# Kernel tuning notes

Measured on AMD Instinct MI355X. Metric: run time of the kernel, lower is better.

Reference implementation:

```python
import jax, jax.numpy as jnp
import numpy as np

B, L, H, NH = 2, 1024, 768, 12
NE, M, NC, CW = 24, 3, 2, 8
BLOCK, NCLS = 64, 97
OFFSET = 1  # bert cls offset


def setup_inputs() -> dict:
    key = jax.random.key(0)
    ks = jax.random.split(key, 10)
    s = 0.02
    return {
        "sequence_output": jax.random.normal(ks[0], (B, L, H), jnp.float32),
        "attention": jax.random.uniform(ks[1], (B, NH, L, L), jnp.float32),
        "mention_starts": jax.random.randint(ks[2], (B, NE, M), 0, L - 2),
        "coref_starts": jax.random.randint(ks[3], (B, NE, NC), 0, L - CW),
        "W_head": jax.random.normal(ks[4], (H, 2 * H), jnp.float32) * s,
        "b_head": jnp.zeros((H,), jnp.float32),
        "W_tail": jax.random.normal(ks[5], (H, 2 * H), jnp.float32) * s,
        "b_tail": jnp.zeros((H,), jnp.float32),
        "W_proj": jax.random.normal(ks[6], (H, H * BLOCK), jnp.float32) * s,
        "W_cls": jax.random.normal(ks[7], (NCLS, H), jnp.float32) * s,
        "b_cls": jnp.zeros((NCLS,), jnp.float32),
    }


def reference(sequence_output, attention, mention_starts, coref_starts,
              W_head, b_head, W_tail, b_tail, W_proj, W_cls, b_cls):
    # ---- get_hrt (NoGraphConv/NoKGEmbedding => graph feats are zeros; residual=True) ----
    p = mention_starts + OFFSET                              # [B,NE,M]
    bidx = jnp.arange(B)[:, None, None]
    m_emb = sequence_output[bidx, p]                         # [B,NE,M,H]
    # attention[i,:,pos] gathered for every mention -> [B,NE,M,NH,L]
    m_att = attention[bidx, :, p]

    # gated coref: gate_score = mean-over-mentions, sum-over-heads, normalized
    att = m_att.mean(2).sum(2)                               # [B,NE,L]
    gate = att / att.sum(-1, keepdims=True)                  # [B,NE,L]

    widx = coref_starts[..., None] + jnp.arange(CW)          # [B,NE,NC,CW]
    gate_g = jnp.take_along_axis(gate[:, :, None, :], widx, axis=-1)   # [B,NE,NC,CW]
    seq_g = sequence_output[jnp.arange(B)[:, None, None, None], widx]  # [B,NE,NC,CW,H]
    coref_emb = (gate_g[..., None] * seq_g).sum(3)           # [B,NE,NC,H]

    # entity embedding: logsumexp over mentions + gated coref vectors
    e_emb = jax.nn.logsumexp(jnp.concatenate([m_emb, coref_emb], axis=2), axis=2)  # [B,NE,H]
    e_att = m_att.mean(2)                                    # [B,NE,NH,L]

    # head-tail localized context: relu((h_att*t_att).sum(heads)), normalize, mix tokens
    ht = jax.nn.relu(jnp.einsum('behl,bfhl->befl', e_att, e_att))      # [B,NE,NE,L]
    ht = ht / (ht.sum(-1, keepdims=True) + 1e-10)
    rs = jnp.einsum('befl,bld->befd', ht, sequence_output)   # [B,NE,NE,H]

    hs = jnp.broadcast_to(e_emb[:, :, None, :], (B, NE, NE, H))
    ts = jnp.broadcast_to(e_emb[:, None, :, :], (B, NE, NE, H))

    # ---- extractors + grouped bilinear + projection + classifier ----
    zh = jnp.tanh(jnp.concatenate([hs, rs], -1) @ W_head.T + b_head)   # [B,NE,NE,H]
    zt = jnp.tanh(jnp.concatenate([ts, rs], -1) @ W_tail.T + b_tail)
    K = H // BLOCK
    b1 = zh.reshape(B, NE, NE, K, BLOCK)
    b2 = zt.reshape(B, NE, NE, K, BLOCK)
    bl = (b1[..., :, None] * b2[..., None, :]).reshape(B, NE, NE, H * BLOCK)
    feature = bl @ W_proj.T                                  # [B,NE,NE,H] (NoAxialTransformer adds zeros)
    logits = feature @ W_cls.T + b_cls                       # [B,NE,NE,NCLS]
    return logits
```

## Files before the change

### kernel.cpp

```cpp
#include <hip/hip_runtime.h>
#include <math.h>

#define BB   2
#define LL   1024
#define HH   768
#define NHH  12
#define NEE  24
#define MMM  3
#define NCC  2
#define CWW  8
#define BLK  64
#define NCLS 97
#define KB   12
#define HB   49152
#define NCP  128
#define NCT  7
#define NEF  1152

typedef unsigned int uint;
typedef unsigned short ushort;
typedef __attribute__((ext_vector_type(8))) short bf16x8;
typedef __attribute__((ext_vector_type(4))) float f32x4;

__device__ __forceinline__ ushort f2bf(float f) {
    uint u = __float_as_uint(f);
    u += 0x7fffu + ((u >> 16) & 1u);
    return (ushort)(u >> 16);
}

__global__ void k_prep(const float* __restrict__ Wc, ushort* __restrict__ wcpack,
                       float* __restrict__ rs, float* __restrict__ out,
                       const float* __restrict__ bc) {
    int bid = blockIdx.x;
    if (bid < 42) {
        int t = bid * 256 + threadIdx.x;
        if (t >= 24 * NCT * 64) return;
        int kc = t / (NCT * 64);
        int r = t % (NCT * 64);
        int ct = r >> 6;
        int lane = r & 63;
        int c = ct * 16 + (lane & 15);
        int k0 = kc * 32 + (lane >> 4) * 8;
        uint u[4] = {0u, 0u, 0u, 0u};
        if (c < NCLS) {
            const float* src = Wc + (size_t)c * HH + k0;
            float4 f0 = *(const float4*)src;
            float4 f1 = *(const float4*)(src + 4);
            u[0] = (uint)f2bf(f0.x) | ((uint)f2bf(f0.y) << 16);
            u[1] = (uint)f2bf(f0.z) | ((uint)f2bf(f0.w) << 16);
            u[2] = (uint)f2bf(f1.x) | ((uint)f2bf(f1.y) << 16);
            u[3] = (uint)f2bf(f1.z) | ((uint)f2bf(f1.w) << 16);
        }
        *(uint4*)(wcpack + (size_t)t * 8) = make_uint4(u[0], u[1], u[2], u[3]);
    } else if (bid < 42 + 3456) {
        int i = (bid - 42) * 256 + threadIdx.x;
        rs[i] = 0.f;
    } else {
        int i = (bid - 3498) * 256 + threadIdx.x;
        if (i < NEF * NCLS) out[i] = bc[i % NCLS];
    }
}

__global__ void k_head(const float* __restrict__ att_in, const float* __restrict__ seq,
                       const int* __restrict__ ms, const int* __restrict__ cs,
                       float* __restrict__ e_att, float* __restrict__ e_emb) {
    __shared__ float es[NHH][LL];
    __shared__ float gs[LL];
    __shared__ float red[16];
    int be = blockIdx.x;
    int b = be / NEE;
    int base = be * MMM;
    int p0 = ms[base + 0] + 1;
    int p1 = ms[base + 1] + 1;
    int p2 = ms[base + 2] + 1;
    int l = threadIdx.x;
    float* eo = e_att + (size_t)be * NHH * LL;
#pragma unroll
    for (int h = 0; h < NHH; h++) {
        const float* basep = att_in + (size_t)(b * NHH + h) * LL * LL;
        float v = (basep[(size_t)p0 * LL + l] + basep[(size_t)p1 * LL + l] +
                   basep[(size_t)p2 * LL + l]) * (1.f / 3.f);
        es[h][l] = v;
        eo[h * LL + l] = v;
    }
    __syncthreads();
    float a = 0.f;
#pragma unroll
    for (int h = 0; h < NHH; h++) a += es[h][l];
    float s = a;
    for (int off = 32; off; off >>= 1) s += __shfl_down(s, off, 64);
    if ((l & 63) == 0) red[l >> 6] = s;
    __syncthreads();
    float tot = 0.f;
#pragma unroll
    for (int i = 0; i < 16; i++) tot += red[i];
    gs[l] = a * (1.f / tot);
    __syncthreads();
    if (l < HH) {
        int d = l;
        int c0 = cs[be * NCC + 0], c1 = cs[be * NCC + 1];
        float v0 = seq[((size_t)b * LL + p0) * HH + d];
        float v1 = seq[((size_t)b * LL + p1) * HH + d];
        float v2 = seq[((size_t)b * LL + p2) * HH + d];
        float s0 = 0.f, s1 = 0.f;
#pragma unroll
        for (int w = 0; w < CWW; w++) {
            s0 += gs[c0 + w] * seq[((size_t)b * LL + c0 + w) * HH + d];
            s1 += gs[c1 + w] * seq[((size_t)b * LL + c1 + w) * HH + d];
        }
        float mx = fmaxf(fmaxf(fmaxf(v0, v1), fmaxf(v2, s0)), s1);
        float se = expf(v0 - mx) + expf(v1 - mx) + expf(v2 - mx) + expf(s0 - mx) + expf(s1 - mx);
        e_emb[(size_t)be * HH + d] = logf(se) + mx;
    }
}

__global__ void k_ht(const float* __restrict__ e_att, float* __restrict__ ht) {
    int blk = blockIdx.x;
    int f = blk % NEE;
    int e = (blk / NEE) % NEE;
    int b = blk / (NEE * NEE);
    const float* ea = e_att + (size_t)(b * NEE + e) * NHH * LL;
    const float* fa = e_att + (size_t)(b * NEE + f) * NHH * LL;
    __shared__ float hts[LL];
    __shared__ float red[4];
    float lsum = 0.f;
    for (int l = threadIdx.x; l < LL; l += blockDim.x) {
        float s = 0.f;
        for (int h = 0; h < NHH; h++) s += ea[h * LL + l] * fa[h * LL + l];
        s = fmaxf(s, 0.f);
        hts[l] = s;
        lsum += s;
    }
    for (int off = 32; off; off >>= 1) lsum += __shfl_down(lsum, off, 64);
    if ((threadIdx.x & 63) == 0) red[threadIdx.x >> 6] = lsum;
    __syncthreads();
    float inv = 1.f / (red[0] + red[1] + red[2] + red[3] + 1e-10f);
    for (int l = threadIdx.x; l < LL; l += blockDim.x)
        ht[(size_t)blk * LL + l] = hts[l] * inv;
}

__global__ void k_mid(const float* __restrict__ seq, const float* __restrict__ ht,
                      float* __restrict__ rs, const float* __restrict__ e_emb,
                      const float* __restrict__ Wh, const float* __restrict__ Wt,
                      float* __restrict__ hsW, float* __restrict__ tsW) {
    __shared__ float As[16][68], Bs[16][68];
    __shared__ float xs[HH];
    int bid = blockIdx.x;
    if (bid < 432) {
        int m0 = (bid % 9) * 64;
        int n0 = ((bid / 9) % 12) * 64;
        int z  = bid / 108;
        int b  = z >> 1;
        int k0base = (z & 1) * 512;
        const float* A  = ht  + (size_t)b * 576 * 1024;
        const float* Bm = seq + (size_t)b * 1024 * 768;
        float* C = rs + (size_t)b * 576 * 768;
        int tx = threadIdx.x & 15, ty = threadIdx.x >> 4;
        int lr = threadIdx.x >> 2;
        int lk = (threadIdx.x & 3) * 4;
        int kr = threadIdx.x >> 4;
        int c4 = (threadIdx.x & 15) * 4;
        float acc[4][4] = {};
        const float* arow = A + (size_t)(m0 + lr) * 1024 + k0base;
        const float* brow = Bm + (size_t)(k0base + kr) * 768 + n0 + c4;
        for (int k0 = 0; k0 < 512; k0 += 16) {
            float4 av = *(const float4*)(arow + k0 + lk);
            float4 bv = *(const float4*)(brow + (size_t)k0 * 768);
            __syncthreads();
            As[lk + 0][lr] = av.x; As[lk + 1][lr] = av.y; As[lk + 2][lr] = av.z; As[lk + 3][lr] = av.w;
            *(float4*)&Bs[kr][c4] = bv;
            __syncthreads();
#pragma unroll
            for (int kk = 0; kk < 16; kk++) {
                float a0 = As[kk][ty * 4 + 0], a1 = As[kk][ty * 4 + 1];
                float a2 = As[kk][ty * 4 + 2], a3 = As[kk][ty * 4 + 3];
                float b0 = Bs[kk][tx * 4 + 0], b1 = Bs[kk][tx * 4 + 1];
                float b2 = Bs[kk][tx * 4 + 2], b3 = Bs[kk][tx * 4 + 3];
                acc[0][0] += a0 * b0; acc[0][1] += a0 * b1; acc[0][2] += a0 * b2; acc[0][3] += a0 * b3;
                acc[1][0] += a1 * b0; acc[1][1] += a1 * b1; acc[1][2] += a1 * b2; acc[1][3] += a1 * b3;
                acc[2][0] += a2 * b0; acc[2][1] += a2 * b1; acc[2][2] += a2 * b2; acc[2][3] += a2 * b3;
                acc[3][0] += a3 * b0; acc[3][1] += a3 * b1; acc[3][2] += a3 * b2; acc[3][3] += a3 * b3;
            }
        }
#pragma unroll
        for (int i = 0; i < 4; i++)
#pragma unroll
            for (int j = 0; j < 4; j++)
                atomicAdd(&C[(size_t)(m0 + ty * 4 + i) * 768 + n0 + tx * 4 + j], acc[i][j]);
    } else {
        int r = bid - 432;
        int m2 = r % 48;
        int which = (r / 48) & 1;
        int chunk = r / 96;
        const float* Wm = which ? Wt : Wh;
        float* outp = which ? tsW : hsW;
        const float* x = e_emb + (size_t)m2 * HH;
        for (int j = threadIdx.x; j < HH; j += 256) xs[j] = x[j];
        __syncthreads();
        int lane = threadIdx.x & 63, w = threadIdx.x >> 6;
        int d0 = chunk * 64 + w * 16;
#pragma unroll 4
        for (int i = 0; i < 16; i++) {
            int d = d0 + i;
            const float* wr = Wm + (size_t)d * (2 * HH);
            float s = 0.f;
#pragma unroll
            for (int jj = 0; jj < 12; jj++) s += xs[lane + jj * 64] * wr[lane + jj * 64];
            for (int off = 32; off; off >>= 1) s += __shfl_down(s, off, 64);
            if (lane == 0) outp[(size_t)m2 * HH + d] = s;
        }
    }
}

__global__ void k_rsw(const float* __restrict__ rs, const float* __restrict__ Wh,
                      const float* __restrict__ Wt, const float* __restrict__ hsW,
                      const float* __restrict__ tsW, const float* __restrict__ bh,
                      const float* __restrict__ bt, ushort* __restrict__ zb) {
    int m0 = blockIdx.x * 64, n0 = blockIdx.y * 64;
    __shared__ float As[16][68], Bs[16][68];
    int tx = threadIdx.x & 15, ty = threadIdx.x >> 4;
    int lr = threadIdx.x >> 2;
    int lk = (threadIdx.x & 3) * 4;
    float acc[4][4] = {};
    int n = n0 + lr;
    const float* brow = (n < HH) ? (Wh + (size_t)n * (2 * HH) + HH)
                                 : (Wt + (size_t)(n - HH) * (2 * HH) + HH);
    const float* arow = rs + (size_t)(m0 + lr) * HH;
    for (int k0 = 0; k0 < HH; k0 += 16) {
        float4 av = *(const float4*)(arow + k0 + lk);
        float4 bv = *(const float4*)(brow + k0 + lk);
        __syncthreads();
        As[lk + 0][lr] = av.x; As[lk + 1][lr] = av.y; As[lk + 2][lr] = av.z; As[lk + 3][lr] = av.w;
        Bs[lk + 0][lr] = bv.x; Bs[lk + 1][lr] = bv.y; Bs[lk + 2][lr] = bv.z; Bs[lk + 3][lr] = bv.w;
        __syncthreads();
#pragma unroll
        for (int kk = 0; kk < 16; kk++) {
            float a0 = As[kk][ty * 4 + 0], a1 = As[kk][ty * 4 + 1];
            float a2 = As[kk][ty * 4 + 2], a3 = As[kk][ty * 4 + 3];
            float b0 = Bs[kk][tx * 4 + 0], b1 = Bs[kk][tx * 4 + 1];
            float b2 = Bs[kk][tx * 4 + 2], b3 = Bs[kk][tx * 4 + 3];
            acc[0][0] += a0 * b0; acc[0][1] += a0 * b1; acc[0][2] += a0 * b2; acc[0][3] += a0 * b3;
            acc[1][0] += a1 * b0; acc[1][1] += a1 * b1; acc[1][2] += a1 * b2; acc[1][3] += a1 * b3;
            acc[2][0] += a2 * b0; acc[2][1] += a2 * b1; acc[2][2] += a2 * b2; acc[2][3] += a2 * b3;
            acc[3][0] += a3 * b0; acc[3][1] += a3 * b1; acc[3][2] += a3 * b2; acc[3][3] += a3 * b3;
        }
    }
    bool isHead = (n0 < HH);
#pragma unroll
    for (int i = 0; i < 4; i++) {
        int m = m0 + ty * 4 + i;
        int bb = m / 576;
        int rr = m % 576;
        int e = rr / NEE, f = rr % NEE;
        const float* addrow = isHead ? (hsW + (size_t)(bb * NEE + e) * HH)
                                     : (tsW + (size_t)(bb * NEE + f) * HH);
        const float* bias = isHead ? bh : bt;
#pragma unroll
        for (int j = 0; j < 4; j++) {
            int nn = n0 + tx * 4 + j;
            int d = isHead ? nn : (nn - HH);
            float v = tanhf(acc[i][j] + addrow[d] + bias[d]);
            zb[(size_t)m * (2 * HH) + nn] = f2bf(v);
        }
    }
}

__global__ void k_wf(const float* __restrict__ Wp, const ushort* __restrict__ wcpack,
                     ushort* __restrict__ bpack) {
    int tid = threadIdx.x;
    int lane = tid & 63, w = tid >> 6;
    int r16 = lane & 15, tt = lane >> 4;
    int n0 = blockIdx.x * 64 + w * 16;
    const float* ap = Wp + (size_t)(tt * 8) * HB + n0 + r16;
    const uint4* wb = (const uint4*)wcpack;

    f32x4 acc[NCT];
    f32x4 zero = {0.f, 0.f, 0.f, 0.f};
#pragma unroll
    for (int ct = 0; ct < NCT; ct++) acc[ct] = zero;

    for (int kc = 0; kc < 24; kc++) {
        const float* a0 = ap + (size_t)(kc * 32) * HB;
        float f[8];
#pragma unroll
        for (int j = 0; j < 8; j++) f[j] = a0[(size_t)j * HB];
        union { bf16x8 v; uint u[4]; } a;
#pragma unroll
        for (int q = 0; q < 4; q++)
            a.u[q] = (__float_as_uint(f[2 * q]) >> 16) |
                     (__float_as_uint(f[2 * q + 1]) & 0xFFFF0000u);
#pragma unroll
        for (int ct = 0; ct < NCT; ct++) {
            union { uint4 q; bf16x8 v; } b;
            b.q = wb[(size_t)(kc * NCT + ct) * 64 + lane];
            acc[ct] = __builtin_amdgcn_mfma_f32_16x16x32_bf16(a.v, b.v, acc[ct], 0, 0, 0);
        }
    }
#pragma unroll
    for (int ct = 0; ct < NCT; ct++) {
        int c = ct * 16 + r16;
#pragma unroll
        for (int r = 0; r < 4; r++) {
            int n = n0 + tt * 4 + r;
            bpack[((size_t)(n >> 3) * NCP + c) * 8 + (n & 7)] = f2bf(acc[ct][r]);
        }
    }
}

#define ZTP 88
#define ZHP 48
__global__ __launch_bounds__(256, 2) void k_logits(const ushort* __restrict__ zb,
                                                   const ushort* __restrict__ bpack,
                                                   float* __restrict__ out) {
    __shared__ ushort zhs[64 * ZHP];
    __shared__ ushort zts[64 * ZTP];
    __shared__ ushort Bls[16384];
    int m0 = blockIdx.x * 64;
    int kb = blockIdx.y;
    int kg = kb >> 1;
    int ihalf = (kb & 1) * 32;
    int tid = threadIdx.x;
    int lane = tid & 63, w = tid >> 6;
    int tt = lane >> 4, r16 = lane & 15;
    int wm = (w & 1) * 32, wn = (w >> 1) * 64;

    {
        int row = tid >> 2, c8 = (tid & 3) * 16;
        const ushort* src = zb + (size_t)(m0 + row) * 1536 + 768 + kg * 64 + c8;
        uint4 v0 = *(const uint4*)src;
        uint4 v1 = *(const uint4*)(src + 8);
        *(uint4*)&zts[row * ZTP + c8] = v0;
        *(uint4*)&zts[row * ZTP + c8 + 8] = v1;
    }
    {
        int row = tid >> 2, c8 = (tid & 3) * 8;
        const ushort* src = zb + (size_t)(m0 + row) * 1536 + kg * 64 + ihalf + c8;
        *(uint4*)&zhs[row * ZHP + c8] = *(const uint4*)src;
    }

    f32x4 acc[2][4];
    f32x4 zero = {0.f, 0.f, 0.f, 0.f};
#pragma unroll
    for (int t = 0; t < 2; t++)
#pragma unroll
        for (int n = 0; n < 4; n++) acc[t][n] = zero;

    const char* bbase = (const char*)bpack + (size_t)kb * 2048 * 256;
    for (int g = 0; g < 16; g++) {
        __syncthreads();
        const char* sb = bbase + (size_t)g * 32768;
#pragma unroll
        for (int q = 0; q < 8; q++) {
            int off = (q * 4 + w) * 1024;
            __builtin_amdgcn_global_load_lds(
                (const __attribute__((address_space(1))) void*)(sb + off + lane * 16),
                (__attribute__((address_space(3))) void*)((char*)Bls + off),
                16, 0, 0);
        }
        __syncthreads();
#pragma unroll
        for (int ks = 0; ks < 4; ks++) {
            int s = g * 4 + ks;
            int il = s >> 1;
            int j0 = (s & 1) * 32;
            bf16x8 af[2];
#pragma unroll
            for (int t = 0; t < 2; t++) {
                int row = wm + t * 16 + r16;
                float zhf = __uint_as_float((uint)zhs[row * ZHP + il] << 16);
                union { bf16x8 v; uint u[4]; } zt8, a;
                zt8.v = *(const bf16x8*)&zts[row * ZTP + j0 + tt * 8];
#pragma unroll
                for (int q = 0; q < 4; q++) {
                    uint p = zt8.u[q];
                    uint lo = __float_as_uint(__uint_as_float(p << 16) * zhf);
                    uint hi = __float_as_uint(__uint_as_float(p & 0xFFFF0000u) * zhf);
                    a.u[q] = (lo >> 16) | (hi & 0xFFFF0000u);
                }
                af[t] = a.v;
            }
#pragma unroll
            for (int n = 0; n < 4; n++) {
                bf16x8 bf = *(const bf16x8*)&Bls[(size_t)((ks * 4 + tt) * NCP + wn + n * 16 + r16) * 8];
                acc[0][n] = __builtin_amdgcn_mfma_f32_16x16x32_bf16(af[0], bf, acc[0][n], 0, 0, 0);
                acc[1][n] = __builtin_amdgcn_mfma_f32_16x16x32_bf16(af[1], bf, acc[1][n], 0, 0, 0);
            }
        }
    }
    int rbase = (lane >> 4) * 4;
#pragma unroll
    for (int t = 0; t < 2; t++)
#pragma unroll
        for (int n = 0; n < 4; n++) {
            int c = wn + n * 16 + r16;
            if (c < NCLS) {
                int row = m0 + wm + t * 16 + rbase;
#pragma unroll
                for (int r = 0; r < 4; r++)
                    atomicAdd(&out[(size_t)(row + r) * NCLS + c], acc[t][n][r]);
            }
        }
}

extern "C" void kernel_launch(void* const* d_in, const int* in_sizes, int n_in,
                              void* d_out, int out_size, void* d_ws, size_t ws_size,
                              hipStream_t stream) {
    const float* seq  = (const float*)d_in[0];
    const float* attn = (const float*)d_in[1];
    const int*   ms   = (const int*)d_in[2];
    const int*   cs   = (const int*)d_in[3];
    const float* Wh   = (const float*)d_in[4];
    const float* bh   = (const float*)d_in[5];
    const float* Wt   = (const float*)d_in[6];
    const float* bt   = (const float*)d_in[7];
    const float* Wp   = (const float*)d_in[8];
    const float* Wc   = (const float*)d_in[9];
    const float* bc   = (const float*)d_in[10];
    float* out = (float*)d_out;

    float* w     = (float*)d_ws;
    float* e_att = w;
    float* ht    = e_att + 589824;
    float* rs    = ht + 1179648;
    float* eemb  = rs + 884736;
    float* hsW   = eemb + 36864;
    float* tsW   = hsW + 36864;
    ushort* bpack  = (ushort*)w;
    ushort* zb     = (ushort*)(w + 3145728);
    ushort* wcpack = (ushort*)(w + 4030464);

    k_prep<<<3935, 256, 0, stream>>>(Wc, wcpack, rs, out, bc);
    k_head<<<BB * NEE, 1024, 0, stream>>>(attn, seq, ms, cs, e_att, eemb);
    k_ht<<<NEF, 256, 0, stream>>>(e_att, ht);
    k_mid<<<432 + 1152, 256, 0, stream>>>(seq, ht, rs, eemb, Wh, Wt, hsW, tsW);
    k_rsw<<<dim3(NEF / 64, 2 * HH / 64), 256, 0, stream>>>(rs, Wh, Wt, hsW, tsW, bh, bt, zb);
    k_wf<<<HB / 64, 256, 0, stream>>>(Wp, wcpack, bpack);
    k_logits<<<dim3(NEF / 64, 24), 256, 0, stream>>>(zb, bpack, out);
}
```

Baseline: 461.4 us.

## Use split-bf16 MFMA for rs and rsW GEMMs and merge launches

Converts the two fp32 SIMT GEMMs (ht@seq and rs@W2) into MFMA bf16 GEMMs, using a hi/lo bf16 split (three MFMAs per tile) to keep near-fp32 accuracy. A front kernel now produces transposed seq and W2 hi/lo copies, fuses head/gating and prep work, and ht is fused with the Wp·Wc fold kernel, cutting the launch count from seven to five. The atomic split-K in rs is removed. The cost is extra conversion passes, larger workspace traffic for the hi/lo copies, and uncached global loads that are not staged through LDS.

```diff
diff --git a/kernel.cpp b/kernel.cpp
--- a/kernel.cpp
+++ b/kernel.cpp
@@ -11,7 +11,6 @@
 #define CWW  8
 #define BLK  64
 #define NCLS 97
-#define KB   12
 #define HB   49152
 #define NCP  128
 #define NCT  7
@@ -28,12 +27,26 @@
     return (ushort)(u >> 16);
 }
 
-__global__ void k_prep(const float* __restrict__ Wc, ushort* __restrict__ wcpack,
-                       float* __restrict__ rs, float* __restrict__ out,
-                       const float* __restrict__ bc) {
+__device__ __forceinline__ void splitbf(float f, ushort& h, ushort& l) {
+    h = f2bf(f);
+    float hf = __uint_as_float((uint)h << 16);
+    l = f2bf(f - hf);
+}
+
+__global__ void k_front(const float* __restrict__ att_in, const float* __restrict__ seq,
+                        const int* __restrict__ ms, const int* __restrict__ cs,
+                        const float* __restrict__ Wc, const float* __restrict__ Wh,
+                        const float* __restrict__ Wt, const float* __restrict__ bc,
+                        float* __restrict__ e_att, float* __restrict__ e_emb,
+                        ushort* __restrict__ wcpack,
+                        ushort* __restrict__ seqThi, ushort* __restrict__ seqTlo,
+                        ushort* __restrict__ W2hi, ushort* __restrict__ W2lo,
+                        float* __restrict__ out) {
+    __shared__ float sm[13328];
     int bid = blockIdx.x;
+    int tid = threadIdx.x;
     if (bid < 42) {
-        int t = bid * 256 + threadIdx.x;
+        int t = bid * 256 + tid;
         if (t >= 24 * NCT * 64) return;
         int kc = t / (NCT * 64);
         int r = t % (NCT * 64);
@@ -52,152 +65,233 @@
             u[3] = (uint)f2bf(f1.z) | ((uint)f2bf(f1.w) << 16);
         }
         *(uint4*)(wcpack + (size_t)t * 8) = make_uint4(u[0], u[1], u[2], u[3]);
-    } else if (bid < 42 + 3456) {
-        int i = (bid - 42) * 256 + threadIdx.x;
-        rs[i] = 0.f;
+    } else if (bid < 479) {
+        int i = (bid - 42) * 256 + tid;
+        if (i < NEF * NCLS) out[i] = bc[i % NCLS];
+    } else if (bid < 527) {
+        float* es = sm;
+        float* gs = sm + 12288;
+        float* red = sm + 13312;
+        int be = bid - 479;
+        int b = be / NEE;
+        int base = be * MMM;
+        int p0 = ms[base + 0] + 1, p1 = ms[base + 1] + 1, p2 = ms[base + 2] + 1;
+        float* eo = e_att + (size_t)be * NHH * LL;
+        for (int h = 0; h < NHH; h++) {
+            const float* basep = att_in + (size_t)(b * NHH + h) * LL * LL;
+#pragma unroll
+            for (int i = 0; i < 4; i++) {
+                int l = tid + i * 256;
+                float v = (basep[(size_t)p0 * LL + l] + basep[(size_t)p1 * LL + l] +
+                           basep[(size_t)p2 * LL + l]) * (1.f / 3.f);
+                es[h * LL + l] = v;
+                eo[h * LL + l] = v;
+            }
+        }
+        __syncthreads();
+        float part = 0.f;
+#pragma unroll
+        for (int i = 0; i < 4; i++) {
+            int l = tid + i * 256;
+            float a = 0.f;
+#pragma unroll
+            for (int h = 0; h < NHH; h++) a += es[h * LL + l];
+            gs[l] = a;
+            part += a;
+        }
+        for (int off = 32; off; off >>= 1) part += __shfl_down(part, off, 64);
+        if ((tid & 63) == 0) red[tid >> 6] = part;
+        __syncthreads();
+        float inv = 1.f / (red[0] + red[1] + red[2] + red[3]);
+#pragma unroll
+        for (int i = 0; i < 4; i++) gs[tid + i * 256] *= inv;
+        __syncthreads();
+        int c0 = cs[be * NCC + 0], c1 = cs[be * NCC + 1];
+        for (int d = tid; d < HH; d += 256) {
+            float v0 = seq[((size_t)b * LL + p0) * HH + d];
+            float v1 = seq[((size_t)b * LL + p1) * HH + d];
+            float v2 = seq[((size_t)b * LL + p2) * HH + d];
+            float s0 = 0.f, s1 = 0.f;
+#pragma unroll
+            for (int w = 0; w < CWW; w++) {
+                s0 += gs[c0 + w] * seq[((size_t)b * LL + c0 + w) * HH + d];
+                s1 += gs[c1 + w] * seq[((size_t)b * LL + c1 + w) * HH + d];
+            }
+            float mx = fmaxf(fmaxf(fmaxf(v0, v1), fmaxf(v2, s0)), s1);
+            float se = expf(v0 - mx) + expf(v1 - mx) + expf(v2 - mx) + expf(s0 - mx) + expf(s1 - mx);
+            e_emb[(size_t)be * HH + d] = logf(se) + mx;
+        }
+    } else if (bid < 911) {
+        float (*tile)[65] = (float(*)[65])sm;
+        int idx = bid - 527;
+        int b = idx / 192;
+        int rem = idx % 192;
+        int l0 = (rem / 12) * 64;
+        int d0 = (rem % 12) * 64;
+        int dq = tid >> 6, dl = tid & 63;
+#pragma unroll 4
+        for (int r = 0; r < 16; r++) {
+            int l_in = r * 4 + dq;
+            tile[l_in][dl] = seq[((size_t)(b * LL + l0 + l_in)) * HH + d0 + dl];
+        }
+        __syncthreads();
+#pragma unroll 4
+        for (int r = 0; r < 16; r++) {
+            int d_out = r * 4 + dq;
+            float v = tile[dl][d_out];
+            ushort h, l;
+            splitbf(v, h, l);
+            size_t o = ((size_t)(b * HH + d0 + d_out)) * LL + l0 + dl;
+            seqThi[o] = h;
+            seqTlo[o] = l;
+        }
     } else {
-        int i = (bid - 3498) * 256 + threadIdx.x;
-        if (i < NEF * NCLS) out[i] = bc[i % NCLS];
-    }
-}
-
-__global__ void k_head(const float* __restrict__ att_in, const float* __restrict__ seq,
-                       const int* __restrict__ ms, const int* __restrict__ cs,
-                       float* __restrict__ e_att, float* __restrict__ e_emb) {
-    __shared__ float es[NHH][LL];
-    __shared__ float gs[LL];
-    __shared__ float red[16];
-    int be = blockIdx.x;
-    int b = be / NEE;
-    int base = be * MMM;
-    int p0 = ms[base + 0] + 1;
-    int p1 = ms[base + 1] + 1;
-    int p2 = ms[base + 2] + 1;
-    int l = threadIdx.x;
-    float* eo = e_att + (size_t)be * NHH * LL;
-#pragma unroll
-    for (int h = 0; h < NHH; h++) {
-        const float* basep = att_in + (size_t)(b * NHH + h) * LL * LL;
-        float v = (basep[(size_t)p0 * LL + l] + basep[(size_t)p1 * LL + l] +
-                   basep[(size_t)p2 * LL + l]) * (1.f / 3.f);
-        es[h][l] = v;
-        eo[h * LL + l] = v;
-    }
-    __syncthreads();
-    float a = 0.f;
-#pragma unroll
-    for (int h = 0; h < NHH; h++) a += es[h][l];
-    float s = a;
-    for (int off = 32; off; off >>= 1) s += __shfl_down(s, off, 64);
-    if ((l & 63) == 0) red[l >> 6] = s;
-    __syncthreads();
-    float tot = 0.f;
-#pragma unroll
-    for (int i = 0; i < 16; i++) tot += red[i];
-    gs[l] = a * (1.f / tot);
-    __syncthreads();
-    if (l < HH) {
-        int d = l;
-        int c0 = cs[be * NCC + 0], c1 = cs[be * NCC + 1];
-        float v0 = seq[((size_t)b * LL + p0) * HH + d];
-        float v1 = seq[((size_t)b * LL + p1) * HH + d];
-        float v2 = seq[((size_t)b * LL + p2) * HH + d];
-        float s0 = 0.f, s1 = 0.f;
-#pragma unroll
-        for (int w = 0; w < CWW; w++) {
-            s0 += gs[c0 + w] * seq[((size_t)b * LL + c0 + w) * HH + d];
-            s1 += gs[c1 + w] * seq[((size_t)b * LL + c1 + w) * HH + d];
-        }
-        float mx = fmaxf(fmaxf(fmaxf(v0, v1), fmaxf(v2, s0)), s1);
-        float se = expf(v0 - mx) + expf(v1 - mx) + expf(v2 - mx) + expf(s0 - mx) + expf(s1 - mx);
-        e_emb[(size_t)be * HH + d] = logf(se) + mx;
-    }
-}
-
-__global__ void k_ht(const float* __restrict__ e_att, float* __restrict__ ht) {
-    int blk = blockIdx.x;
-    int f = blk % NEE;
-    int e = (blk / NEE) % NEE;
-    int b = blk / (NEE * NEE);
-    const float* ea = e_att + (size_t)(b * NEE + e) * NHH * LL;
-    const float* fa = e_att + (size_t)(b * NEE + f) * NHH * LL;
+        int idx = bid - 911;
+#pragma unroll
+        for (int rr = 0; rr < 4; rr++) {
+            int n = idx * 4 + rr;
+            const float* src = (n < HH) ? (Wh + (size_t)n * (2 * HH) + HH)
+                                        : (Wt + (size_t)(n - HH) * (2 * HH) + HH);
+            for (int k = tid; k < HH; k += 256) {
+                ushort h, l;
+                splitbf(src[k], h, l);
+                W2hi[(size_t)n * HH + k] = h;
+                W2lo[(size_t)n * HH + k] = l;
+            }
+        }
+    }
+}
+
+__global__ void k_htwf(const float* __restrict__ e_att, const float* __restrict__ Wp,
+                       const ushort* __restrict__ wcpack, ushort* __restrict__ hthi,
+                       ushort* __restrict__ htlo, ushort* __restrict__ bpack) {
     __shared__ float hts[LL];
     __shared__ float red[4];
-    float lsum = 0.f;
-    for (int l = threadIdx.x; l < LL; l += blockDim.x) {
-        float s = 0.f;
-        for (int h = 0; h < NHH; h++) s += ea[h * LL + l] * fa[h * LL + l];
-        s = fmaxf(s, 0.f);
-        hts[l] = s;
-        lsum += s;
-    }
-    for (int off = 32; off; off >>= 1) lsum += __shfl_down(lsum, off, 64);
-    if ((threadIdx.x & 63) == 0) red[threadIdx.x >> 6] = lsum;
-    __syncthreads();
-    float inv = 1.f / (red[0] + red[1] + red[2] + red[3] + 1e-10f);
-    for (int l = threadIdx.x; l < LL; l += blockDim.x)
-        ht[(size_t)blk * LL + l] = hts[l] * inv;
-}
-
-__global__ void k_mid(const float* __restrict__ seq, const float* __restrict__ ht,
-                      float* __restrict__ rs, const float* __restrict__ e_emb,
-                      const float* __restrict__ Wh, const float* __restrict__ Wt,
-                      float* __restrict__ hsW, float* __restrict__ tsW) {
-    __shared__ float As[16][68], Bs[16][68];
+    int bid = blockIdx.x;
+    int tid = threadIdx.x;
+    int lane = tid & 63, w = tid >> 6;
+    if (bid < 768) {
+        int r16 = lane & 15, tt = lane >> 4;
+        int n0 = bid * 64 + w * 16;
+        const float* ap = Wp + (size_t)(tt * 8) * HB + n0 + r16;
+        const uint4* wb = (const uint4*)wcpack;
+        f32x4 acc[NCT];
+        f32x4 zero = {0.f, 0.f, 0.f, 0.f};
+#pragma unroll
+        for (int ct = 0; ct < NCT; ct++) acc[ct] = zero;
+        for (int kc = 0; kc < 24; kc++) {
+            const float* a0 = ap + (size_t)(kc * 32) * HB;
+            float f[8];
+#pragma unroll
+            for (int j = 0; j < 8; j++) f[j] = a0[(size_t)j * HB];
+            union { bf16x8 v; uint u[4]; } a;
+#pragma unroll
+            for (int q = 0; q < 4; q++)
+                a.u[q] = (__float_as_uint(f[2 * q]) >> 16) |
+                         (__float_as_uint(f[2 * q + 1]) & 0xFFFF0000u);
+#pragma unroll
+            for (int ct = 0; ct < NCT; ct++) {
+                union { uint4 q; bf16x8 v; } b;
+                b.q = wb[(size_t)(kc * NCT + ct) * 64 + lane];
+                acc[ct] = __builtin_amdgcn_mfma_f32_16x16x32_bf16(a.v, b.v, acc[ct], 0, 0, 0);
+            }
+        }
+#pragma unroll
+        for (int ct = 0; ct < NCT; ct++) {
+            int c = ct * 16 + r16;
+#pragma unroll
+            for (int r = 0; r < 4; r++) {
+                int n = n0 + tt * 4 + r;
+                bpack[((size_t)(n >> 3) * NCP + c) * 8 + (n & 7)] = f2bf(acc[ct][r]);
+            }
+        }
+    } else {
+        int blk = bid - 768;
+        int f = blk % NEE;
+        int e = (blk / NEE) % NEE;
+        int b = blk / (NEE * NEE);
+        const float* ea = e_att + (size_t)(b * NEE + e) * NHH * LL;
+        const float* fa = e_att + (size_t)(b * NEE + f) * NHH * LL;
+        float lsum = 0.f;
+        for (int l = tid; l < LL; l += 256) {
+            float s = 0.f;
+            for (int h = 0; h < NHH; h++) s += ea[h * LL + l] * fa[h * LL + l];
+            s = fmaxf(s, 0.f);
+            hts[l] = s;
+            lsum += s;
+        }
+        for (int off = 32; off; off >>= 1) lsum += __shfl_down(lsum, off, 64);
+        if ((tid & 63) == 0) red[tid >> 6] = lsum;
+        __syncthreads();
+        float inv = 1.f / (red[0] + red[1] + red[2] + red[3] + 1e-10f);
+        for (int l = tid; l < LL; l += 256) {
+            ushort h, lo;
+            splitbf(hts[l] * inv, h, lo);
+            hthi[(size_t)blk * LL + l] = h;
+            htlo[(size_t)blk * LL + l] = lo;
+        }
+    }
+}
+
+__global__ void k_mid(const ushort* __restrict__ seqThi, const ushort* __restrict__ seqTlo,
+                      const ushort* __restrict__ hthi, const ushort* __restrict__ htlo,
+                      const float* __restrict__ e_emb, const float* __restrict__ Wh,
+                      const float* __restrict__ Wt, ushort* __restrict__ rshi,
+                      ushort* __restrict__ rslo, float* __restrict__ hsW,
+                      float* __restrict__ tsW) {
     __shared__ float xs[HH];
     int bid = blockIdx.x;
-    if (bid < 432) {
-        int m0 = (bid % 9) * 64;
-        int n0 = ((bid / 9) % 12) * 64;
-        int z  = bid / 108;
-        int b  = z >> 1;
-        int k0base = (z & 1) * 512;
-        const float* A  = ht  + (size_t)b * 576 * 1024;
-        const float* Bm = seq + (size_t)b * 1024 * 768;
-        float* C = rs + (size_t)b * 576 * 768;
-        int tx = threadIdx.x & 15, ty = threadIdx.x >> 4;
-        int lr = threadIdx.x >> 2;
-        int lk = (threadIdx.x & 3) * 4;
-        int kr = threadIdx.x >> 4;
-        int c4 = (threadIdx.x & 15) * 4;
-        float acc[4][4] = {};
-        const float* arow = A + (size_t)(m0 + lr) * 1024 + k0base;
-        const float* brow = Bm + (size_t)(k0base + kr) * 768 + n0 + c4;
-        for (int k0 = 0; k0 < 512; k0 += 16) {
-            float4 av = *(const float4*)(arow + k0 + lk);
-            float4 bv = *(const float4*)(brow + (size_t)k0 * 768);
-            __syncthreads();
-            As[lk + 0][lr] = av.x; As[lk + 1][lr] = av.y; As[lk + 2][lr] = av.z; As[lk + 3][lr] = av.w;
-            *(float4*)&Bs[kr][c4] = bv;
-            __syncthreads();
-#pragma unroll
-            for (int kk = 0; kk < 16; kk++) {
-                float a0 = As[kk][ty * 4 + 0], a1 = As[kk][ty * 4 + 1];
-                float a2 = As[kk][ty * 4 + 2], a3 = As[kk][ty * 4 + 3];
-                float b0 = Bs[kk][tx * 4 + 0], b1 = Bs[kk][tx * 4 + 1];
-                float b2 = Bs[kk][tx * 4 + 2], b3 = Bs[kk][tx * 4 + 3];
-                acc[0][0] += a0 * b0; acc[0][1] += a0 * b1; acc[0][2] += a0 * b2; acc[0][3] += a0 * b3;
-                acc[1][0] += a1 * b0; acc[1][1] += a1 * b1; acc[1][2] += a1 * b2; acc[1][3] += a1 * b3;
-                acc[2][0] += a2 * b0; acc[2][1] += a2 * b1; acc[2][2] += a2 * b2; acc[2][3] += a2 * b3;
-                acc[3][0] += a3 * b0; acc[3][1] += a3 * b1; acc[3][2] += a3 * b2; acc[3][3] += a3 * b3;
-            }
-        }
-#pragma unroll
-        for (int i = 0; i < 4; i++)
-#pragma unroll
-            for (int j = 0; j < 4; j++)
-                atomicAdd(&C[(size_t)(m0 + ty * 4 + i) * 768 + n0 + tx * 4 + j], acc[i][j]);
+    int tid = threadIdx.x;
+    int lane = tid & 63, w = tid >> 6;
+    if (bid < 216) {
+        int b = bid / 108;
+        int rem = bid % 108;
+        int m0 = (rem / 12) * 64;
+        int n0 = (rem % 12) * 64;
+        int r16 = lane & 15, tt = lane >> 4;
+        const ushort* Ah = hthi + (size_t)(b * 576 + m0 + w * 16 + r16) * LL;
+        const ushort* Al = htlo + (size_t)(b * 576 + m0 + w * 16 + r16) * LL;
+        const ushort* Bh0 = seqThi + (size_t)(b * HH + n0 + r16) * LL;
+        const ushort* Bl0 = seqTlo + (size_t)(b * HH + n0 + r16) * LL;
+        f32x4 acc[4];
+        f32x4 zero = {0.f, 0.f, 0.f, 0.f};
+#pragma unroll
+        for (int nt = 0; nt < 4; nt++) acc[nt] = zero;
+        for (int kc = 0; kc < 32; kc++) {
+            int ko = kc * 32 + tt * 8;
+            bf16x8 ah = *(const bf16x8*)(Ah + ko);
+            bf16x8 al = *(const bf16x8*)(Al + ko);
+#pragma unroll
+            for (int nt = 0; nt < 4; nt++) {
+                bf16x8 bh = *(const bf16x8*)(Bh0 + (size_t)nt * 16 * LL + ko);
+                bf16x8 bl = *(const bf16x8*)(Bl0 + (size_t)nt * 16 * LL + ko);
+                acc[nt] = __builtin_amdgcn_mfma_f32_16x16x32_bf16(ah, bh, acc[nt], 0, 0, 0);
+                acc[nt] = __builtin_amdgcn_mfma_f32_16x16x32_bf16(ah, bl, acc[nt], 0, 0, 0);
+                acc[nt] = __builtin_amdgcn_mfma_f32_16x16x32_bf16(al, bh, acc[nt], 0, 0, 0);
+            }
+        }
+#pragma unroll
+        for (int nt = 0; nt < 4; nt++) {
+#pragma unroll
+            for (int r = 0; r < 4; r++) {
+                int m = b * 576 + m0 + w * 16 + tt * 4 + r;
+                int d = n0 + nt * 16 + r16;
+                ushort h, l;
+                splitbf(acc[nt][r], h, l);
+                rshi[(size_t)m * HH + d] = h;
+                rslo[(size_t)m * HH + d] = l;
+            }
+        }
     } else {
-        int r = bid - 432;
+        int r = bid - 216;
         int m2 = r % 48;
         int which = (r / 48) & 1;
         int chunk = r / 96;
         const float* Wm = which ? Wt : Wh;
         float* outp = which ? tsW : hsW;
         const float* x = e_emb + (size_t)m2 * HH;
-        for (int j = threadIdx.x; j < HH; j += 256) xs[j] = x[j];
-        __syncthreads();
-        int lane = threadIdx.x & 63, w = threadIdx.x >> 6;
+        for (int j = tid; j < HH; j += 256) xs[j] = x[j];
+        __syncthreads();
         int d0 = chunk * 64 + w * 16;
 #pragma unroll 4
         for (int i = 0; i < 16; i++) {
@@ -212,97 +306,52 @@
     }
 }
 
-__global__ void k_rsw(const float* __restrict__ rs, const float* __restrict__ Wh,
-                      const float* __restrict__ Wt, const float* __restrict__ hsW,
-                      const float* __restrict__ tsW, const float* __restrict__ bh,
-                      const float* __restrict__ bt, ushort* __restrict__ zb) {
+__global__ void k_rsw(const ushort* __restrict__ rshi, const ushort* __restrict__ rslo,
+                      const ushort* __restrict__ W2hi, const ushort* __restrict__ W2lo,
+                      const float* __restrict__ hsW, const float* __restrict__ tsW,
+                      const float* __restrict__ bh, const float* __restrict__ bt,
+                      ushort* __restrict__ zb) {
     int m0 = blockIdx.x * 64, n0 = blockIdx.y * 64;
-    __shared__ float As[16][68], Bs[16][68];
-    int tx = threadIdx.x & 15, ty = threadIdx.x >> 4;
-    int lr = threadIdx.x >> 2;
-    int lk = (threadIdx.x & 3) * 4;
-    float acc[4][4] = {};
-    int n = n0 + lr;
-    const float* brow = (n < HH) ? (Wh + (size_t)n * (2 * HH) + HH)
-                                 : (Wt + (size_t)(n - HH) * (2 * HH) + HH);
-    const float* arow = rs + (size_t)(m0 + lr) * HH;
-    for (int k0 = 0; k0 < HH; k0 += 16) {
-        float4 av = *(const float4*)(arow + k0 + lk);
-        float4 bv = *(const float4*)(brow + k0 + lk);
-        __syncthreads();
-        As[lk + 0][lr] = av.x; As[lk + 1][lr] = av.y; As[lk + 2][lr] = av.z; As[lk + 3][lr] = av.w;
-        Bs[lk + 0][lr] = bv.x; Bs[lk + 1][lr] = bv.y; Bs[lk + 2][lr] = bv.z; Bs[lk + 3][lr] = bv.w;
-        __syncthreads();
-#pragma unroll
-        for (int kk = 0; kk < 16; kk++) {
-            float a0 = As[kk][ty * 4 + 0], a1 = As[kk][ty * 4 + 1];
-            float a2 = As[kk][ty * 4 + 2], a3 = As[kk][ty * 4 + 3];
-            float b0 = Bs[kk][tx * 4 + 0], b1 = Bs[kk][tx * 4 + 1];
-            float b2 = Bs[kk][tx * 4 + 2], b3 = Bs[kk][tx * 4 + 3];
-            acc[0][0] += a0 * b0; acc[0][1] += a0 * b1; acc[0][2] += a0 * b2; acc[0][3] += a0 * b3;
-            acc[1][0] += a1 * b0; acc[1][1] += a1 * b1; acc[1][2] += a1 * b2; acc[1][3] += a1 * b3;
-            acc[2][0] += a2 * b0; acc[2][1] += a2 * b1; acc[2][2] += a2 * b2; acc[2][3] += a2 * b3;
-            acc[3][0] += a3 * b0; acc[3][1] += a3 * b1; acc[3][2] += a3 * b2; acc[3][3] += a3 * b3;
-        }
-    }
-    bool isHead = (n0 < HH);
-#pragma unroll
-    for (int i = 0; i < 4; i++) {
-        int m = m0 + ty * 4 + i;
-        int bb = m / 576;
-        int rr = m % 576;
-        int e = rr / NEE, f = rr % NEE;
-        const float* addrow = isHead ? (hsW + (size_t)(bb * NEE + e) * HH)
-                                     : (tsW + (size_t)(bb * NEE + f) * HH);
-        const float* bias = isHead ? bh : bt;
-#pragma unroll
-        for (int j = 0; j < 4; j++) {
-            int nn = n0 + tx * 4 + j;
-            int d = isHead ? nn : (nn - HH);
-            float v = tanhf(acc[i][j] + addrow[d] + bias[d]);
-            zb[(size_t)m * (2 * HH) + nn] = f2bf(v);
-        }
-    }
-}
-
-__global__ void k_wf(const float* __restrict__ Wp, const ushort* __restrict__ wcpack,
-                     ushort* __restrict__ bpack) {
     int tid = threadIdx.x;
     int lane = tid & 63, w = tid >> 6;
     int r16 = lane & 15, tt = lane >> 4;
-    int n0 = blockIdx.x * 64 + w * 16;
-    const float* ap = Wp + (size_t)(tt * 8) * HB + n0 + r16;
-    const uint4* wb = (const uint4*)wcpack;
-
-    f32x4 acc[NCT];
+    const ushort* Ah = rshi + (size_t)(m0 + w * 16 + r16) * HH;
+    const ushort* Al = rslo + (size_t)(m0 + w * 16 + r16) * HH;
+    const ushort* Bh0 = W2hi + (size_t)(n0 + r16) * HH;
+    const ushort* Bl0 = W2lo + (size_t)(n0 + r16) * HH;
+    f32x4 acc[4];
     f32x4 zero = {0.f, 0.f, 0.f, 0.f};
 #pragma unroll
-    for (int ct = 0; ct < NCT; ct++) acc[ct] = zero;
-
+    for (int nt = 0; nt < 4; nt++) acc[nt] = zero;
     for (int kc = 0; kc < 24; kc++) {
-        const float* a0 = ap + (size_t)(kc * 32) * HB;
-        float f[8];
-#pragma unroll
-        for (int j = 0; j < 8; j++) f[j] = a0[(size_t)j * HB];
-        union { bf16x8 v; uint u[4]; } a;
-#pragma unroll
-        for (int q = 0; q < 4; q++)
-            a.u[q] = (__float_as_uint(f[2 * q]) >> 16) |
-                     (__float_as_uint(f[2 * q + 1]) & 0xFFFF0000u);
-#pragma unroll
-        for (int ct = 0; ct < NCT; ct++) {
-            union { uint4 q; bf16x8 v; } b;
-            b.q = wb[(size_t)(kc * NCT + ct) * 64 + lane];
-            acc[ct] = __builtin_amdgcn_mfma_f32_16x16x32_bf16(a.v, b.v, acc[ct], 0, 0, 0);
-        }
-    }
-#pragma unroll
-    for (int ct = 0; ct < NCT; ct++) {
-        int c = ct * 16 + r16;
+        int ko = kc * 32 + tt * 8;
+        bf16x8 ah = *(const bf16x8*)(Ah + ko);
+        bf16x8 al = *(const bf16x8*)(Al + ko);
+#pragma unroll
+        for (int nt = 0; nt < 4; nt++) {
+            bf16x8 vbh = *(const bf16x8*)(Bh0 + (size_t)nt * 16 * HH + ko);
+            bf16x8 vbl = *(const bf16x8*)(Bl0 + (size_t)nt * 16 * HH + ko);
+            acc[nt] = __builtin_amdgcn_mfma_f32_16x16x32_bf16(ah, vbh, acc[nt], 0, 0, 0);
+            acc[nt] = __builtin_amdgcn_mfma_f32_16x16x32_bf16(ah, vbl, acc[nt], 0, 0, 0);
+            acc[nt] = __builtin_amdgcn_mfma_f32_16x16x32_bf16(al, vbh, acc[nt], 0, 0, 0);
+        }
+    }
+    bool isHead = (n0 < HH);
+    const float* bias = isHead ? bh : bt;
+#pragma unroll
+    for (int nt = 0; nt < 4; nt++) {
 #pragma unroll
         for (int r = 0; r < 4; r++) {
-            int n = n0 + tt * 4 + r;
-            bpack[((size_t)(n >> 3) * NCP + c) * 8 + (n & 7)] = f2bf(acc[ct][r]);
+            int m = m0 + w * 16 + tt * 4 + r;
+            int n = n0 + nt * 16 + r16;
+            int bb = m / 576;
+            int rr = m % 576;
+            int e = rr / NEE, f = rr % NEE;
+            int d = isHead ? n : (n - HH);
+            const float* addrow = isHead ? (hsW + (size_t)(bb * NEE + e) * HH)
+                                         : (tsW + (size_t)(bb * NEE + f) * HH);
+            float v = tanhf(acc[nt][r] + addrow[d] + bias[d]);
+            zb[(size_t)m * (2 * HH) + n] = f2bf(v);
         }
     }
 }
@@ -420,20 +469,26 @@
 
     float* w     = (float*)d_ws;
     float* e_att = w;
-    float* ht    = e_att + 589824;
-    float* rs    = ht + 1179648;
-    float* eemb  = rs + 884736;
+    float* eemb  = e_att + 589824;
     float* hsW   = eemb + 36864;
     float* tsW   = hsW + 36864;
-    ushort* bpack  = (ushort*)w;
-    ushort* zb     = (ushort*)(w + 3145728);
-    ushort* wcpack = (ushort*)(w + 4030464);
-
-    k_prep<<<3935, 256, 0, stream>>>(Wc, wcpack, rs, out, bc);
-    k_head<<<BB * NEE, 1024, 0, stream>>>(attn, seq, ms, cs, e_att, eemb);
-    k_ht<<<NEF, 256, 0, stream>>>(e_att, ht);
-    k_mid<<<432 + 1152, 256, 0, stream>>>(seq, ht, rs, eemb, Wh, Wt, hsW, tsW);
-    k_rsw<<<dim3(NEF / 64, 2 * HH / 64), 256, 0, stream>>>(rs, Wh, Wt, hsW, tsW, bh, bt, zb);
-    k_wf<<<HB / 64, 256, 0, stream>>>(Wp, wcpack, bpack);
-    k_logits<<<dim3(NEF / 64, 24), 256, 0, stream>>>(zb, bpack, out);
-}
+    ushort* seqThi = (ushort*)(tsW + 36864);
+    ushort* seqTlo = seqThi + 1572864;
+    ushort* W2hi   = seqTlo + 1572864;
+    ushort* W2lo   = W2hi + 1179648;
+    ushort* hthi   = W2lo + 1179648;
+    ushort* htlo   = hthi + 1179648;
+    ushort* rshi   = htlo + 1179648;
+    ushort* rslo   = rshi + 884736;
+    ushort* zb     = rslo + 884736;
+    ushort* wcpack = zb + 1769472;
+    ushort* bpack  = wcpack + 86016;
+
+    k_front<<<1295, 256, 0, stream>>>(attn, seq, ms, cs, Wc, Wh, Wt, bc,
+                                      e_att, eemb, wcpack, seqThi, seqTlo, W2hi, W2lo, out);
+    k_htwf<<<1920, 256, 0, stream>>>(e_att, Wp, wcpack, hthi, htlo, bpack);
+    k_mid<<<1368, 256, 0, stream>>>(seqThi, seqTlo, hthi, htlo, eemb, Wh, Wt,
+                                    rshi, rslo, hsW, tsW);
+    k_rsw<<<dim3(18, 24), 256, 0, stream>>>(rshi, rslo, W2hi, W2lo, hsW, tsW, bh, bt, zb);
+    k_logits<<<dim3(18, 24), 256, 0, stream>>>(zb, bpack, out);
+}
```

New measurement: 447.8 us. 1.03x faster.
